# Kernel optimization log

Hardware: AMD Instinct MI355X
Metric: run time of the kernel (lower is better)

Reference implementation:

```python
import jax, jax.numpy as jnp
import numpy as np

NEG_SLOPE = 0.2  # PyG GATConv default leaky_relu slope

def gat_conv(x, src, dst, W, att_src, att_dst, bias, concat):
    # x: [N, F_in]; W: [F_in, H*D]; att_*: [H, D]; edges src->dst
    N = x.shape[0]
    H, D = att_src.shape
    h = (x @ W).reshape(N, H, D)                      # [N, H, D]
    a_src = (h * att_src[None]).sum(-1)               # [N, H]
    a_dst = (h * att_dst[None]).sum(-1)               # [N, H]
    e = jax.nn.leaky_relu(a_src[src] + a_dst[dst], NEG_SLOPE)  # [E, H]
    # segment softmax over incoming edges of each destination node
    emax = jax.ops.segment_max(e, dst, num_segments=N)          # [N, H]
    emax = jnp.where(jnp.isfinite(emax), emax, 0.0)
    ex = jnp.exp(e - emax[dst])                                  # [E, H]
    denom = jax.ops.segment_sum(ex, dst, num_segments=N)        # [N, H]
    alpha = ex / (denom[dst] + 1e-16)                            # [E, H]
    msg = h[src] * alpha[:, :, None]                             # [E, H, D]
    out = jax.ops.segment_sum(msg, dst, num_segments=N)          # [N, H, D]
    out = out.reshape(N, H * D) if concat else out.mean(axis=1)
    return out + bias

def setup_inputs() -> dict:
    key = jax.random.key(0)
    ks = jax.random.split(key, 10)
    N, F_in, E, H, D, C = 100000, 128, 3200000, 8, 8, 7
    x = jax.random.normal(ks[0], (N, F_in), jnp.float32)
    edge_index = jax.random.randint(ks[1], (2, E), 0, N, jnp.int64)
    W1 = jax.random.normal(ks[2], (F_in, H * D), jnp.float32) / np.sqrt(F_in)
    att_src1 = jax.random.normal(ks[3], (H, D), jnp.float32) / np.sqrt(D)
    att_dst1 = jax.random.normal(ks[4], (H, D), jnp.float32) / np.sqrt(D)
    b1 = jax.random.normal(ks[5], (H * D,), jnp.float32) * 0.01
    W2 = jax.random.normal(ks[6], (H * D, C), jnp.float32) / np.sqrt(H * D)
    att_src2 = jax.random.normal(ks[7], (1, C), jnp.float32) / np.sqrt(C)
    att_dst2 = jax.random.normal(ks[8], (1, C), jnp.float32) / np.sqrt(C)
    b2 = jax.random.normal(ks[9], (C,), jnp.float32) * 0.01
    return {"x": x, "edge_index": edge_index, "W1": W1, "att_src1": att_src1,
            "att_dst1": att_dst1, "b1": b1, "W2": W2, "att_src2": att_src2,
            "att_dst2": att_dst2, "b2": b2}

def reference(x, edge_index, W1, att_src1, att_dst1, b1, W2, att_src2, att_dst2, b2):
    N = x.shape[0]
    # PyG GATConv add_self_loops=True
    loop = jnp.arange(N, dtype=edge_index.dtype)
    src = jnp.concatenate([edge_index[0], loop])
    dst = jnp.concatenate([edge_index[1], loop])
    # eval mode: dropouts are no-ops
    h = gat_conv(x, src, dst, W1, att_src1, att_dst1, b1, concat=True)
    emb = h
    h = jax.nn.elu(h)
    logits = gat_conv(h, src, dst, W2, att_src2, att_dst2, b2, concat=False)
    return emb, jax.nn.log_softmax(logits, axis=1)
```

## Files before the change

### kernel.cpp

```cpp
#include <hip/hip_runtime.h>
#include <hip/hip_bf16.h>
#include <math.h>

#define F_IN 128
#define HD   64
#define NH   8
#define DH   8
#define NC   7

__device__ __forceinline__ float lrelu(float e) { return fmaxf(e, 0.2f * e); }
__device__ __forceinline__ ushort f2bf(float f) {
    unsigned u = __float_as_uint(f);
    unsigned rounded = u + 0x7FFF + ((u >> 16) & 1);
    return (ushort)(rounded >> 16);
}

__global__ __launch_bounds__(256) void k_gemm1h(
    const float* __restrict__ x, const float* __restrict__ W1,
    const float* __restrict__ att_src, const float* __restrict__ att_dst,
    ushort* __restrict__ h1b, float* __restrict__ a_src, float* __restrict__ a_dst,
    int N, int GB,
    const int* __restrict__ dstArr, int* __restrict__ deg, int* __restrict__ rank,
    long E)
{
    __shared__ float sW[F_IN * HD];
    __shared__ float sX[64 * F_IN];
    int t = threadIdx.x;
    int bid = blockIdx.x;

    if (bid % 3 != 0) {
        long hb = (long)(bid / 3) * 2 + (bid % 3) - 1;
        long stride = (long)(2 * GB) * 256;
        for (long i = hb * 256 + t; i < E; i += stride)
            rank[i] = atomicAdd(&deg[dstArr[i]], 1);
        return;
    }

    int gb = bid / 3;
    int lane = t & 63;
    int wave = t >> 6;

    {
        float4 wv[8], xv[8];
        int r0b = gb * 64;
        #pragma unroll
        for (int i = 0; i < 8; ++i) {
            int ch = i * 256 + t;
            wv[i] = *(const float4*)(W1 + ch * 4);
            int rr = r0b + (ch >> 5);
            if (rr >= N) rr = N - 1;
            xv[i] = *(const float4*)(x + (size_t)rr * F_IN + ((ch & 31) << 2));
        }
        #pragma unroll
        for (int i = 0; i < 8; ++i) {
            int ch = i * 256 + t;
            *(float4*)(sW + ch * 4) = wv[i];
            *(float4*)(sX + ch * 4) = xv[i];
        }
    }
    float asv = att_src[lane];
    float adv = att_dst[lane];
    __syncthreads();

    int base = gb * 64 + wave * 16;

    for (int it = 0; it < 2; ++it) {
        int r0 = base + it * 8;
        if (r0 >= N) break;
        int nr = N - r0; if (nr > 8) nr = 8;
        int lr = wave * 16 + it * 8;
        const float* xr[8];
        #pragma unroll
        for (int r = 0; r < 8; ++r) xr[r] = sX + (lr + r) * F_IN;

        float acc[8];
        #pragma unroll
        for (int r = 0; r < 8; ++r) acc[r] = 0.f;

        #pragma unroll 4
        for (int k4 = 0; k4 < F_IN / 4; ++k4) {
            float4 xv[8];
            #pragma unroll
            for (int r = 0; r < 8; ++r)
                xv[r] = *(const float4*)(xr[r] + k4 * 4);
            #pragma unroll
            for (int kk = 0; kk < 4; ++kk) {
                float sw = sW[(k4 * 4 + kk) * HD + lane];
                acc[0] += ((const float*)&xv[0])[kk] * sw;
                acc[1] += ((const float*)&xv[1])[kk] * sw;
                acc[2] += ((const float*)&xv[2])[kk] * sw;
                acc[3] += ((const float*)&xv[3])[kk] * sw;
                acc[4] += ((const float*)&xv[4])[kk] * sw;
                acc[5] += ((const float*)&xv[5])[kk] * sw;
                acc[6] += ((const float*)&xv[6])[kk] * sw;
                acc[7] += ((const float*)&xv[7])[kk] * sw;
            }
        }
        #pragma unroll
        for (int r = 0; r < 8; ++r) {
            if (r < nr) {
                int row = r0 + r;
                float a = acc[r];
                h1b[(size_t)row * HD + lane] = f2bf(a);
                float vs = a * asv;
                float vd = a * adv;
                #pragma unroll
                for (int o = 4; o > 0; o >>= 1) {
                    vs += __shfl_down(vs, o, 8);
                    vd += __shfl_down(vd, o, 8);
                }
                if ((lane & 7) == 0) {
                    int h = lane >> 3;
                    a_src[row * NH + h] = vs;
                    a_dst[row * NH + h] = vd;
                }
            }
        }
    }
}

__global__ __launch_bounds__(256) void k_bsum(
    const int* __restrict__ deg, int* __restrict__ bsum, int N)
{
    __shared__ int s[256];
    int t = threadIdx.x;
    int i = blockIdx.x * 256 + t;
    s[t] = (i < N) ? deg[i] : 0;
    __syncthreads();
    #pragma unroll
    for (int o = 128; o > 0; o >>= 1) {
        if (t < o) s[t] += s[t + o];
        __syncthreads();
    }
    if (t == 0) bsum[blockIdx.x] = s[0];
}

__global__ __launch_bounds__(512) void k_scan_bsum(
    const int* __restrict__ bsum, int* __restrict__ bexc, int NB)
{
    __shared__ int s[512];
    int t = threadIdx.x;
    s[t] = (t < NB) ? bsum[t] : 0;
    __syncthreads();
    for (int o = 1; o < 512; o <<= 1) {
        int v = (t >= o) ? s[t - o] : 0;
        __syncthreads();
        s[t] += v;
        __syncthreads();
    }
    if (t < NB) bexc[t] = (t == 0) ? 0 : s[t - 1];
}

__global__ __launch_bounds__(256) void k_rowptr(
    const int* __restrict__ deg, const int* __restrict__ bexc,
    int* __restrict__ rowptr, int N, int Etot)
{
    __shared__ int s[256];
    int t = threadIdx.x;
    int i = blockIdx.x * 256 + t;
    int v = (i < N) ? deg[i] : 0;
    s[t] = v;
    __syncthreads();
    for (int o = 1; o < 256; o <<= 1) {
        int u = (t >= o) ? s[t - o] : 0;
        __syncthreads();
        s[t] += u;
        __syncthreads();
    }
    if (i < N) rowptr[i] = bexc[blockIdx.x] + s[t] - v;
    if (i == 0) rowptr[N] = Etot;
}

__global__ __launch_bounds__(256) void k_fill(
    const int* __restrict__ src, const int* __restrict__ dst,
    const int* __restrict__ rank, const int* __restrict__ rowptr,
    int* __restrict__ csr, long E)
{
    long i = (long)blockIdx.x * 256 + threadIdx.x;
    if (i >= E) return;
    csr[rowptr[dst[i]] + rank[i]] = src[i];
}

__global__ __launch_bounds__(256) void k_gather1(
    const int* __restrict__ rowptr, const int* __restrict__ csr,
    const ushort* __restrict__ h1b, const float* __restrict__ a_src,
    const float* __restrict__ a_dst, float* __restrict__ agg, int N)
{
    const uint* __restrict__ h1u = (const uint*)h1b;
    int wave = threadIdx.x >> 6, lane = threadIdx.x & 63;
    int d = blockIdx.x * 4 + wave;
    if (d >= N) return;
    int e = lane >> 3;
    int h = lane & 7;

    float adst = a_dst[d * NH + h];
    float ws = __expf(lrelu(a_src[d * NH + h] + adst));
    float wsum = (e == 0) ? ws : 0.f;

    float ax0 = 0.f, ay0 = 0.f, ax1 = 0.f, ay1 = 0.f;
    float ax2 = 0.f, ay2 = 0.f, ax3 = 0.f, ay3 = 0.f;
    if (e == 0) {
        size_t b = (size_t)d * 32 + h * 4;
        uint u0 = h1u[b], u1 = h1u[b + 1], u2 = h1u[b + 2], u3 = h1u[b + 3];
        ax0 = ws * __uint_as_float(u0 << 16); ay0 = ws * __uint_as_float(u0 & 0xFFFF0000u);
        ax1 = ws * __uint_as_float(u1 << 16); ay1 = ws * __uint_as_float(u1 & 0xFFFF0000u);
        ax2 = ws * __uint_as_float(u2 << 16); ay2 = ws * __uint_as_float(u2 & 0xFFFF0000u);
        ax3 = ws * __uint_as_float(u3 << 16); ay3 = ws * __uint_as_float(u3 & 0xFFFF0000u);
    }

    int jb = rowptr[d], je = rowptr[d + 1];
    int  idx0   = jb + e;
    bool v_cur  = idx0 < je;
    int  sl_cur = v_cur ? csr[idx0] : d;
    float as_cur = a_src[sl_cur * NH + h];

    for (int j0 = jb; j0 < je; j0 += 8) {
        int  idxn  = j0 + 8 + e;
        bool v_n   = idxn < je;
        int  sl_n  = v_n ? csr[idxn] : d;
        float as_n = a_src[sl_n * NH + h];

        float w = v_cur ? __expf(lrelu(as_cur + adst)) : 0.f;
        wsum += w;
        size_t b = (size_t)sl_cur * 32 + h * 4;
        uint u0 = h1u[b], u1 = h1u[b + 1], u2 = h1u[b + 2], u3 = h1u[b + 3];
        ax0 += w * __uint_as_float(u0 << 16); ay0 += w * __uint_as_float(u0 & 0xFFFF0000u);
        ax1 += w * __uint_as_float(u1 << 16); ay1 += w * __uint_as_float(u1 & 0xFFFF0000u);
        ax2 += w * __uint_as_float(u2 << 16); ay2 += w * __uint_as_float(u2 & 0xFFFF0000u);
        ax3 += w * __uint_as_float(u3 << 16); ay3 += w * __uint_as_float(u3 & 0xFFFF0000u);

        sl_cur = sl_n; as_cur = as_n; v_cur = v_n;
    }

    #pragma unroll
    for (int o = 8; o <= 32; o <<= 1) {
        wsum += __shfl_xor(wsum, o, 64);
        ax0 += __shfl_xor(ax0, o, 64); ay0 += __shfl_xor(ay0, o, 64);
        ax1 += __shfl_xor(ax1, o, 64); ay1 += __shfl_xor(ay1, o, 64);
        ax2 += __shfl_xor(ax2, o, 64); ay2 += __shfl_xor(ay2, o, 64);
        ax3 += __shfl_xor(ax3, o, 64); ay3 += __shfl_xor(ay3, o, 64);
    }
    if (e == 0) {
        float winv = 1.f / (wsum + 1e-16f);
        float* op = agg + (size_t)d * HD + h * 8;
        *(float4*)(op)     = make_float4(ax0 * winv, ay0 * winv, ax1 * winv, ay1 * winv);
        *(float4*)(op + 4) = make_float4(ax2 * winv, ay2 * winv, ax3 * winv, ay3 * winv);
    }
}

__global__ __launch_bounds__(256) void k_node2(
    const float* __restrict__ agg1, const float* __restrict__ b1,
    const float* __restrict__ W2, const float* __restrict__ att_s2,
    const float* __restrict__ att_d2, float* __restrict__ emb_out,
    float* __restrict__ h2p, float* __restrict__ a_src2, float* __restrict__ a_dst2,
    int N)
{
    __shared__ float sW[HD * NC];
    __shared__ float sb[HD];
    __shared__ float sas[NC], sad[NC];
    int t = threadIdx.x;
    for (int i = t; i < HD * NC; i += 256) sW[i] = W2[i];
    if (t < HD) sb[t] = b1[t];
    if (t < NC) { sas[t] = att_s2[t]; sad[t] = att_d2[t]; }
    __syncthreads();
    int n = blockIdx.x * 256 + t;
    if (n >= N) return;
    const float* ag = agg1 + (size_t)n * HD;
    float* eo = emb_out + (size_t)n * HD;
    float acc[NC];
    #pragma unroll
    for (int c = 0; c < NC; ++c) acc[c] = 0.f;
    #pragma unroll 8
    for (int k = 0; k < HD; ++k) {
        float v = ag[k] + sb[k];
        eo[k] = v;
        float xv = v > 0.f ? v : expm1f(v);
        #pragma unroll
        for (int c = 0; c < NC; ++c) acc[c] += xv * sW[k * NC + c];
    }
    float as = 0.f, ad = 0.f;
    float* hp = h2p + (size_t)n * 8;
    #pragma unroll
    for (int c = 0; c < NC; ++c) {
        hp[c] = acc[c];
        as += acc[c] * sas[c];
        ad += acc[c] * sad[c];
    }
    hp[7] = 0.f;
    a_src2[n] = as;
    a_dst2[n] = ad;
}

__global__ __launch_bounds__(256) void k_gather2(
    const int* __restrict__ rowptr, const int* __restrict__ csr,
    const float* __restrict__ h2p, const float* __restrict__ a_src2,
    const float* __restrict__ a_dst2, const float* __restrict__ b2,
    float* __restrict__ out, int N)
{
    int t = threadIdx.x;
    int wave = t >> 6, lane = t & 63;
    int g = lane >> 3;
    int c = lane & 7;
    int n = blockIdx.x * 4 + wave;
    if (n >= N) return;
    float ad = a_dst2[n];
    float w = __expf(lrelu(a_src2[n] + ad));
    float acc  = (g == 0) ? w * h2p[(size_t)n * 8 + c] : 0.f;
    float wsum = (g == 0) ? w : 0.f;
    int jb = rowptr[n], je = rowptr[n + 1];

    int  idx0  = jb + g;
    bool v_cur = idx0 < je;
    int  s_cur = v_cur ? csr[idx0] : n;

    for (int j = jb; j < je; j += 8) {
        int  idxn  = j + 8 + g;
        bool v_n   = idxn < je;
        int  s_n   = v_n ? csr[idxn] : n;
        float ww = v_cur ? __expf(lrelu(a_src2[s_cur] + ad)) : 0.f;
        acc += ww * h2p[(size_t)s_cur * 8 + c];
        wsum += ww;
        s_cur = s_n; v_cur = v_n;
    }
    #pragma unroll
    for (int o = 32; o >= 8; o >>= 1) {
        acc  += __shfl_xor(acc, o, 64);
        wsum += __shfl_xor(wsum, o, 64);
    }
    float l = (c < NC) ? (acc / (wsum + 1e-16f) + b2[c]) : -1e30f;
    float m = l;
    #pragma unroll
    for (int o = 4; o > 0; o >>= 1) m = fmaxf(m, __shfl_xor(m, o, 8));
    float ex = (c < NC) ? __expf(l - m) : 0.f;
    float s8 = ex;
    #pragma unroll
    for (int o = 4; o > 0; o >>= 1) s8 += __shfl_xor(s8, o, 8);
    if (g == 0 && c < NC) out[(size_t)n * NC + c] = l - m - logf(s8);
}

extern "C" void kernel_launch(void* const* d_in, const int* in_sizes, int n_in,
                              void* d_out, int out_size, void* d_ws, size_t ws_size,
                              hipStream_t stream)
{
    const float* x       = (const float*)d_in[0];
    const int*   ei      = (const int*)d_in[1];
    const float* W1      = (const float*)d_in[2];
    const float* att_s1  = (const float*)d_in[3];
    const float* att_d1  = (const float*)d_in[4];
    const float* b1      = (const float*)d_in[5];
    const float* W2      = (const float*)d_in[6];
    const float* att_s2  = (const float*)d_in[7];
    const float* att_d2  = (const float*)d_in[8];
    const float* b2      = (const float*)d_in[9];

    const int  N = in_sizes[0] / F_IN;
    const long E = (long)in_sizes[1] / 2;
    const int* src = ei;
    const int* dst = ei + E;

    const int Npad  = (N + 3) & ~3;
    const int Np1p  = (N + 4) & ~3;
    const long Epad = (E + 3) & ~3;

    int* deg    = (int*)d_ws;
    int* rowptr = deg + Npad;
    int* bexc   = rowptr + Np1p;
    int* bsum   = bexc + 512;
    int* csr    = bsum + 512;
    ushort* h1b   = (ushort*)(csr + Epad);
    float* a_src1 = (float*)(h1b + (size_t)Npad * HD);
    float* a_dst1 = a_src1 + (size_t)N * NH;
    float* agg1   = a_dst1 + (size_t)N * NH;
    float* h2p    = agg1 + (size_t)N * HD;
    float* a_src2 = h2p + (size_t)N * 8;
    float* a_dst2 = a_src2 + Npad;
    float* wsend  = a_dst2 + Npad;
    int* rank = (E <= (long)N * HD) ? (int*)agg1 : (int*)wsend;

    hipMemsetAsync(deg, 0, (size_t)Npad * sizeof(int), stream);

    const int NB = (N + 255) / 256;
    const int GB = (N + 63) / 64;
    dim3 b256(256);

    k_gemm1h<<<dim3(3 * GB), b256, 0, stream>>>(
        x, W1, att_s1, att_d1, h1b, a_src1, a_dst1, N, GB,
        dst, deg, rank, E);
    k_bsum<<<dim3(NB), b256, 0, stream>>>(deg, bsum, N);
    k_scan_bsum<<<dim3(1), dim3(512), 0, stream>>>(bsum, bexc, NB);
    k_rowptr<<<dim3(NB), b256, 0, stream>>>(deg, bexc, rowptr, N, (int)E);
    k_fill<<<dim3((unsigned)((E + 255) / 256)), b256, 0, stream>>>(
        src, dst, rank, rowptr, csr, E);

    k_gather1<<<dim3((N + 3) / 4), b256, 0, stream>>>(
        rowptr, csr, h1b, a_src1, a_dst1, agg1, N);

    float* emb = (float*)d_out;
    float* lsm = emb + (size_t)N * HD;
    k_node2<<<dim3(NB), b256, 0, stream>>>(
        agg1, b1, W2, att_s2, att_d2, emb, h2p, a_src2, a_dst2, N);

    k_gather2<<<dim3((N + 3) / 4), b256, 0, stream>>>(
        rowptr, csr, h2p, a_src2, a_dst2, b2, lsm, N);
}
```

Measured before the change: 656.9 us.

## Drop LDS staging of x in gemm1, transpose W tile, vectorize degree atomics

```diff
diff --git a/kernel.cpp b/kernel.cpp
--- a/kernel.cpp
+++ b/kernel.cpp
@@ -23,16 +23,25 @@
     const int* __restrict__ dstArr, int* __restrict__ deg, int* __restrict__ rank,
     long E)
 {
-    __shared__ float sW[F_IN * HD];
-    __shared__ float sX[64 * F_IN];
+    __shared__ float sWt[32][64][4];
     int t = threadIdx.x;
     int bid = blockIdx.x;
 
     if (bid % 3 != 0) {
         long hb = (long)(bid / 3) * 2 + (bid % 3) - 1;
-        long stride = (long)(2 * GB) * 256;
-        for (long i = hb * 256 + t; i < E; i += stride)
-            rank[i] = atomicAdd(&deg[dstArr[i]], 1);
+        long base = hb * 1024 + (long)t * 4;
+        if (base >= E) return;
+        if (base + 3 < E) {
+            int4 d4 = *(const int4*)(dstArr + base);
+            int r0_ = atomicAdd(&deg[d4.x], 1);
+            int r1_ = atomicAdd(&deg[d4.y], 1);
+            int r2_ = atomicAdd(&deg[d4.z], 1);
+            int r3_ = atomicAdd(&deg[d4.w], 1);
+            *(int4*)(rank + base) = make_int4(r0_, r1_, r2_, r3_);
+        } else {
+            for (long i = base; i < E; ++i)
+                rank[i] = atomicAdd(&deg[dstArr[i]], 1);
+        }
         return;
     }
 
@@ -40,80 +49,65 @@
     int lane = t & 63;
     int wave = t >> 6;
 
-    {
-        float4 wv[8], xv[8];
-        int r0b = gb * 64;
-        #pragma unroll
-        for (int i = 0; i < 8; ++i) {
-            int ch = i * 256 + t;
-            wv[i] = *(const float4*)(W1 + ch * 4);
-            int rr = r0b + (ch >> 5);
-            if (rr >= N) rr = N - 1;
-            xv[i] = *(const float4*)(x + (size_t)rr * F_IN + ((ch & 31) << 2));
-        }
-        #pragma unroll
-        for (int i = 0; i < 8; ++i) {
-            int ch = i * 256 + t;
-            *(float4*)(sW + ch * 4) = wv[i];
-            *(float4*)(sX + ch * 4) = xv[i];
-        }
+    for (int i = t; i < 2048; i += 256) {
+        float4 wv = *(const float4*)(W1 + i * 4);
+        int k  = i >> 4;
+        int c0 = (i * 4) & 63;
+        int k4 = k >> 2, kj = k & 3;
+        sWt[k4][c0 + 0][kj] = wv.x;
+        sWt[k4][c0 + 1][kj] = wv.y;
+        sWt[k4][c0 + 2][kj] = wv.z;
+        sWt[k4][c0 + 3][kj] = wv.w;
     }
     float asv = att_src[lane];
     float adv = att_dst[lane];
     __syncthreads();
 
-    int base = gb * 64 + wave * 16;
-
-    for (int it = 0; it < 2; ++it) {
-        int r0 = base + it * 8;
-        if (r0 >= N) break;
-        int nr = N - r0; if (nr > 8) nr = 8;
-        int lr = wave * 16 + it * 8;
-        const float* xr[8];
+    int r0 = gb * 64 + wave * 16;
+    if (r0 >= N) return;
+
+    int rbase[16];
+    #pragma unroll
+    for (int r = 0; r < 16; ++r) {
+        int rr = r0 + r; if (rr >= N) rr = N - 1;
+        rbase[r] = __builtin_amdgcn_readfirstlane(rr) * F_IN;
+    }
+
+    float acc[16];
+    #pragma unroll
+    for (int r = 0; r < 16; ++r) acc[r] = 0.f;
+
+    #pragma unroll 2
+    for (int k4 = 0; k4 < 32; ++k4) {
+        float4 wt = *(const float4*)&sWt[k4][lane][0];
         #pragma unroll
-        for (int r = 0; r < 8; ++r) xr[r] = sX + (lr + r) * F_IN;
-
-        float acc[8];
-        #pragma unroll
-        for (int r = 0; r < 8; ++r) acc[r] = 0.f;
-
-        #pragma unroll 4
-        for (int k4 = 0; k4 < F_IN / 4; ++k4) {
-            float4 xv[8];
+        for (int r = 0; r < 16; ++r) {
+            float4 xv = *(const float4*)(x + (size_t)rbase[r] + k4 * 4);
+            acc[r] += xv.x * wt.x;
+            acc[r] += xv.y * wt.y;
+            acc[r] += xv.z * wt.z;
+            acc[r] += xv.w * wt.w;
+        }
+    }
+
+    int nr = N - r0; if (nr > 16) nr = 16;
+    #pragma unroll
+    for (int r = 0; r < 16; ++r) {
+        if (r < nr) {
+            int row = r0 + r;
+            float a = acc[r];
+            h1b[(size_t)row * HD + lane] = f2bf(a);
+            float vs = a * asv;
+            float vd = a * adv;
             #pragma unroll
-            for (int r = 0; r < 8; ++r)
-                xv[r] = *(const float4*)(xr[r] + k4 * 4);
-            #pragma unroll
-            for (int kk = 0; kk < 4; ++kk) {
-                float sw = sW[(k4 * 4 + kk) * HD + lane];
-                acc[0] += ((const float*)&xv[0])[kk] * sw;
-                acc[1] += ((const float*)&xv[1])[kk] * sw;
-                acc[2] += ((const float*)&xv[2])[kk] * sw;
-                acc[3] += ((const float*)&xv[3])[kk] * sw;
-                acc[4] += ((const float*)&xv[4])[kk] * sw;
-                acc[5] += ((const float*)&xv[5])[kk] * sw;
-                acc[6] += ((const float*)&xv[6])[kk] * sw;
-                acc[7] += ((const float*)&xv[7])[kk] * sw;
+            for (int o = 4; o > 0; o >>= 1) {
+                vs += __shfl_down(vs, o, 8);
+                vd += __shfl_down(vd, o, 8);
             }
-        }
-        #pragma unroll
-        for (int r = 0; r < 8; ++r) {
-            if (r < nr) {
-                int row = r0 + r;
-                float a = acc[r];
-                h1b[(size_t)row * HD + lane] = f2bf(a);
-                float vs = a * asv;
-                float vd = a * adv;
-                #pragma unroll
-                for (int o = 4; o > 0; o >>= 1) {
-                    vs += __shfl_down(vs, o, 8);
-                    vd += __shfl_down(vd, o, 8);
-                }
-                if ((lane & 7) == 0) {
-                    int h = lane >> 3;
-                    a_src[row * NH + h] = vs;
-                    a_dst[row * NH + h] = vd;
-                }
+            if ((lane & 7) == 0) {
+                int h = lane >> 3;
+                a_src[row * NH + h] = vs;
+                a_dst[row * NH + h] = vd;
             }
         }
     }
```

Result: slower. 702.4 us (+6.9%).
